# Kernel optimization log

Hardware: AMD Instinct MI355X
Metric: run time of the kernel (lower is better)

The kernel has to match this reference:

```python
import jax, jax.numpy as jnp
import numpy as np

GROUPS = 8
EPS = 1e-5


def group_norm(x, gamma, beta):
    b, c, h, w = x.shape
    xg = x.reshape(b, GROUPS, c // GROUPS, h, w)
    mu = jnp.mean(xg, axis=(2, 3, 4), keepdims=True)
    var = jnp.mean((xg - mu) ** 2, axis=(2, 3, 4), keepdims=True)
    xn = ((xg - mu) * jax.lax.rsqrt(var + EPS)).reshape(b, c, h, w)
    return xn * gamma[None, :, None, None] + beta[None, :, None, None]


def setup_inputs() -> dict:
    key = jax.random.key(0)
    ks = jax.random.split(key, 4)
    b, c, h, w = 4, 64, 64, 64
    x = jax.random.normal(ks[0], (b, c, h, w), dtype=jnp.float32)
    gamma = jnp.ones((c,), dtype=jnp.float32)
    beta = jnp.zeros((c,), dtype=jnp.float32)
    w_qkv = jax.random.normal(ks[1], (3 * c, c), dtype=jnp.float32) * (1.0 / np.sqrt(c))
    b_qkv = jnp.zeros((3 * c,), dtype=jnp.float32)
    w_proj = jax.random.normal(ks[2], (c, c), dtype=jnp.float32) * (1.0 / np.sqrt(c))
    b_proj = jnp.zeros((c,), dtype=jnp.float32)
    return {"x": x, "gamma": gamma, "beta": beta, "w_qkv": w_qkv,
            "b_qkv": b_qkv, "w_proj": w_proj, "b_proj": b_proj}


def reference(x, gamma, beta, w_qkv, b_qkv, w_proj, b_proj):
    b, c, h, w = x.shape
    xn = group_norm(x, gamma, beta)
    # 1x1 conv == per-pixel linear: [b,3c,h,w]
    qkv = jnp.einsum('oc,bchw->bohw', w_qkv, xn) + b_qkv[None, :, None, None]
    q, k, v = jnp.split(qkv, 3, axis=1)
    # flatten spatial -> tokens: [b, hw, c]
    def tok(t):
        return t.reshape(b, c, h * w).transpose(0, 2, 1)
    q, k, v = tok(q), tok(k), tok(v)
    scale = c ** (-0.5)
    attn = jnp.einsum('bqc,bkc->bqk', q, k) * scale  # [b, hw, hw]
    attn = jax.nn.softmax(attn, axis=-1)
    out = jnp.einsum('bqk,bkc->bqc', attn, v)  # [b, hw, c]
    out = out.transpose(0, 2, 1).reshape(b, c, h, w)
    out = jnp.einsum('oc,bchw->bohw', w_proj, out) + b_proj[None, :, None, None]
    return out + x
```

## Files before the change

### kernel.cpp

```cpp
#include <hip/hip_runtime.h>

typedef __bf16 bf16x8 __attribute__((ext_vector_type(8)));
typedef __bf16 bf16x4 __attribute__((ext_vector_type(4)));
typedef float  f32x4  __attribute__((ext_vector_type(4)));

#define GLD_LDS16(gsrc, ldst) \
  __builtin_amdgcn_global_load_lds((const __attribute__((address_space(1))) void*)(gsrc), \
                                   (__attribute__((address_space(3))) void*)(ldst), 16, 0, 0)

__global__ __launch_bounds__(256) void gn_partial_k(const float* __restrict__ x,
                                                    float* __restrict__ partial) {
  __shared__ float red[2][4];
  const int t = threadIdx.x;
  const float4* base = (const float4*)(x + (size_t)blockIdx.x * 4096);
  float s = 0.f, sq = 0.f;
#pragma unroll
  for (int kk = 0; kk < 4; ++kk) {
    float4 v = base[t + kk * 256];
    s  += (v.x + v.y) + (v.z + v.w);
    sq += (v.x * v.x + v.y * v.y) + (v.z * v.z + v.w * v.w);
  }
#pragma unroll
  for (int o = 32; o >= 1; o >>= 1) {
    s  += __shfl_down(s, o, 64);
    sq += __shfl_down(sq, o, 64);
  }
  if ((t & 63) == 0) { red[0][t >> 6] = s; red[1][t >> 6] = sq; }
  __syncthreads();
  if (t == 0) {
    float S  = (red[0][0] + red[0][1]) + (red[0][2] + red[0][3]);
    float SQ = (red[1][0] + red[1][1]) + (red[1][2] + red[1][3]);
    partial[blockIdx.x * 2]     = S;
    partial[blockIdx.x * 2 + 1] = SQ;
  }
}

__global__ void gn_final_k(const float* __restrict__ partial, float* __restrict__ stats) {
  const int t = threadIdx.x;
  if (t < 32) {
    float S = 0.f, SQ = 0.f;
#pragma unroll
    for (int i = 0; i < 8; ++i) {
      S  += partial[(t * 8 + i) * 2];
      SQ += partial[(t * 8 + i) * 2 + 1];
    }
    float mean = S * (1.f / 32768.f);
    float var  = SQ * (1.f / 32768.f) - mean * mean;
    stats[t * 2]     = mean;
    stats[t * 2 + 1] = rsqrtf(fmaxf(var, 0.f) + 1e-5f);
  }
}

__global__ __launch_bounds__(192) void qkv_k(const float* __restrict__ x,
                                             const float* __restrict__ stats,
                                             const float* __restrict__ gamma,
                                             const float* __restrict__ beta,
                                             const float* __restrict__ w_qkv,
                                             const float* __restrict__ b_qkv,
                                             __bf16* __restrict__ qo,
                                             __bf16* __restrict__ ko,
                                             __bf16* __restrict__ vto) {
  __shared__ float xn_lds[32 * 68];
  __shared__ float v_lds[64 * 33];
  const int t  = threadIdx.x;
  const int b  = blockIdx.x >> 7;
  const int s0 = (blockIdx.x & 127) * 32;

  for (int idx = t; idx < 2048; idx += 192) {
    int c = idx >> 5, px = idx & 31;
    float v  = x[((size_t)(b * 64 + c)) * 4096 + s0 + px];
    int   g2 = (b * 8 + (c >> 3)) * 2;
    xn_lds[px * 68 + c] = (v - stats[g2]) * stats[g2 + 1] * gamma[c] + beta[c];
  }
  float4 wr[16];
  const float4* wrow = (const float4*)(w_qkv + t * 64);
#pragma unroll
  for (int i = 0; i < 16; ++i) wr[i] = wrow[i];
  const float bias = b_qkv[t];
  __syncthreads();

  for (int px = 0; px < 32; ++px) {
    const float4* xr = (const float4*)&xn_lds[px * 68];
    float a0 = bias, a1 = 0.f, a2 = 0.f, a3 = 0.f;
#pragma unroll
    for (int i = 0; i < 16; i += 4) {
      float4 x0 = xr[i], x1 = xr[i + 1], x2 = xr[i + 2], x3 = xr[i + 3];
      a0 += wr[i    ].x * x0.x + wr[i    ].y * x0.y + wr[i    ].z * x0.z + wr[i    ].w * x0.w;
      a1 += wr[i + 1].x * x1.x + wr[i + 1].y * x1.y + wr[i + 1].z * x1.z + wr[i + 1].w * x1.w;
      a2 += wr[i + 2].x * x2.x + wr[i + 2].y * x2.y + wr[i + 2].z * x2.z + wr[i + 2].w * x2.w;
      a3 += wr[i + 3].x * x3.x + wr[i + 3].y * x3.y + wr[i + 3].z * x3.z + wr[i + 3].w * x3.w;
    }
    float acc = (a0 + a1) + (a2 + a3);
    if (t < 64)
      qo[((size_t)b * 4096 + s0 + px) * 64 + t] = (__bf16)(acc * 0.125f);
    else if (t < 128)
      ko[((size_t)b * 4096 + s0 + px) * 64 + (t - 64)] = (__bf16)acc;
    else
      v_lds[(t - 128) * 33 + px] = acc;
  }
  __syncthreads();
  for (int u = t; u < 2048; u += 192) {
    int rowc = u >> 5, px = u & 31;
    vto[((size_t)(b * 64 + rowc)) * 4096 + s0 + px] = (__bf16)v_lds[rowc * 33 + px];
  }
}

__global__ __launch_bounds__(512, 2) void attn_k(const __bf16* __restrict__ q,
                                                 const __bf16* __restrict__ k,
                                                 const __bf16* __restrict__ vt,
                                                 __bf16* __restrict__ opart,
                                                 float* __restrict__ mlpart) {
  __shared__ __bf16 k_lds[3][4096];
  __shared__ __bf16 v_lds[3][4096];
  __shared__ __bf16 p_lds[8][2048];
  const int tid  = threadIdx.x;
  const int lane = tid & 63, w = tid >> 6;
  const int row  = lane & 15, grp = lane >> 4;

  const int blk  = blockIdx.x;
  const int xcd  = blk & 7;
  const int b    = xcd >> 1;
  const int rest = blk >> 3;
  const int seg  = rest >> 3;
  const int qblk = (rest & 7) | ((xcd & 1) << 3);
  const int q0   = qblk * 256 + w * 32;
  const int j0b  = seg * 512;

  const __bf16* qp = q  + (size_t)b * 4096 * 64;
  const __bf16* kp = k  + (size_t)b * 4096 * 64;
  const __bf16* vp = vt + (size_t)b * 64 * 4096;

  bf16x8 qf[2][2];
#pragma unroll
  for (int rt = 0; rt < 2; ++rt)
#pragma unroll
    for (int kc = 0; kc < 2; ++kc)
      qf[rt][kc] = *(const bf16x8*)(qp + (size_t)(q0 + rt * 16 + row) * 64 + kc * 32 + grp * 8);
  __builtin_amdgcn_sched_barrier(0);

  f32x4 acc[2][4];
#pragma unroll
  for (int rt = 0; rt < 2; ++rt)
#pragma unroll
    for (int dt = 0; dt < 4; ++dt) acc[rt][dt] = (f32x4){0.f, 0.f, 0.f, 0.f};
  float m[2] = {-1e30f, -1e30f}, l[2] = {0.f, 0.f};

  const int soff = tid * 16;
  const int sj = soff >> 7;
  const int sc = ((soff >> 4) & 7) ^ (sj & 7);

  auto stage = [&](int buf, int j0) {
    GLD_LDS16(kp + (size_t)(j0 + sj) * 64 + sc * 8, (char*)(&k_lds[buf][0]) + soff);
    GLD_LDS16(vp + (size_t)sj * 4096 + j0 + sc * 8, (char*)(&v_lds[buf][0]) + soff);
  };

  stage(0, j0b);
  stage(1, j0b + 64);

  char* const pbase = (char*)&p_lds[w][0];
  const int swz = (row & 7) << 3;

#pragma unroll
  for (int kt = 0; kt < 8; ++kt) {
    const int cur = kt % 3;
    if (kt < 6) stage((kt + 2) % 3, j0b + (kt + 2) * 64);

    if (kt < 6)       asm volatile("s_waitcnt vmcnt(4)" ::: "memory");
    else if (kt == 6) asm volatile("s_waitcnt vmcnt(2)" ::: "memory");
    else              asm volatile("s_waitcnt vmcnt(0)" ::: "memory");
    __builtin_amdgcn_s_barrier();

    const char* kbase = (const char*)&k_lds[cur][0];
    const char* vbase = (const char*)&v_lds[cur][0];

    f32x4 sa[2][4];
#pragma unroll
    for (int rt = 0; rt < 2; ++rt)
#pragma unroll
      for (int jt = 0; jt < 4; ++jt) sa[rt][jt] = (f32x4){0.f, 0.f, 0.f, 0.f};
    __builtin_amdgcn_s_setprio(1);
#pragma unroll
    for (int jt = 0; jt < 4; ++jt) {
      const int jr = jt * 16 + row;
      bf16x8 kf0 = *(const bf16x8*)(kbase + jr * 128 + ((grp ^ (row & 7)) << 4));
      bf16x8 kf1 = *(const bf16x8*)(kbase + jr * 128 + (((4 + grp) ^ (row & 7)) << 4));
      sa[0][jt] = __builtin_amdgcn_mfma_f32_16x16x32_bf16(kf0, qf[0][0], sa[0][jt], 0, 0, 0);
      sa[1][jt] = __builtin_amdgcn_mfma_f32_16x16x32_bf16(kf0, qf[1][0], sa[1][jt], 0, 0, 0);
      sa[0][jt] = __builtin_amdgcn_mfma_f32_16x16x32_bf16(kf1, qf[0][1], sa[0][jt], 0, 0, 0);
      sa[1][jt] = __builtin_amdgcn_mfma_f32_16x16x32_bf16(kf1, qf[1][1], sa[1][jt], 0, 0, 0);
    }
    __builtin_amdgcn_s_setprio(0);

#pragma unroll
    for (int rt = 0; rt < 2; ++rt) {
      float t0 = fmaxf(fmaxf(sa[rt][0][0], sa[rt][0][1]), fmaxf(sa[rt][0][2], sa[rt][0][3]));
      float t1 = fmaxf(fmaxf(sa[rt][1][0], sa[rt][1][1]), fmaxf(sa[rt][1][2], sa[rt][1][3]));
      float t2 = fmaxf(fmaxf(sa[rt][2][0], sa[rt][2][1]), fmaxf(sa[rt][2][2], sa[rt][2][3]));
      float t3 = fmaxf(fmaxf(sa[rt][3][0], sa[rt][3][1]), fmaxf(sa[rt][3][2], sa[rt][3][3]));
      float tmax = fmaxf(fmaxf(t0, t1), fmaxf(t2, t3));
      tmax = fmaxf(tmax, __shfl_xor(tmax, 16, 64));
      tmax = fmaxf(tmax, __shfl_xor(tmax, 32, 64));
      float mn = fmaxf(m[rt], tmax);
      float sf = __expf(m[rt] - mn);
      m[rt] = mn;
      float ls = 0.f;
#pragma unroll
      for (int jt = 0; jt < 4; ++jt) {
        float p0 = __expf(sa[rt][jt][0] - mn);
        float p1 = __expf(sa[rt][jt][1] - mn);
        float p2 = __expf(sa[rt][jt][2] - mn);
        float p3 = __expf(sa[rt][jt][3] - mn);
        ls += (p0 + p1) + (p2 + p3);
        bf16x4 pv = {(__bf16)p0, (__bf16)p1, (__bf16)p2, (__bf16)p3};
        *(bf16x4*)(pbase + ((rt * 16 + row) << 7) + ((((grp << 2) + (jt << 4)) ^ swz) << 1)) = pv;
      }
      l[rt] = l[rt] * sf + ls;
#pragma unroll
      for (int dt = 0; dt < 4; ++dt) {
        acc[rt][dt][0] *= sf; acc[rt][dt][1] *= sf;
        acc[rt][dt][2] *= sf; acc[rt][dt][3] *= sf;
      }
    }
    asm volatile("s_waitcnt lgkmcnt(0)" ::: "memory");

    __builtin_amdgcn_s_setprio(1);
#pragma unroll
    for (int kc = 0; kc < 2; ++kc) {
      const int koff = (((kc << 5) + (grp << 3)) ^ swz) << 1;
      bf16x8 af0 = *(const bf16x8*)(pbase + (row << 7) + koff);
      bf16x8 af1 = *(const bf16x8*)(pbase + ((16 + row) << 7) + koff);
#pragma unroll
      for (int dt = 0; dt < 4; ++dt) {
        const int dr = dt * 16 + row;
        bf16x8 vf = *(const bf16x8*)(vbase + dr * 128 + ((((kc << 2) + grp) ^ (row & 7)) << 4));
        acc[0][dt] = __builtin_amdgcn_mfma_f32_16x16x32_bf16(vf, af0, acc[0][dt], 0, 0, 0);
        acc[1][dt] = __builtin_amdgcn_mfma_f32_16x16x32_bf16(vf, af1, acc[1][dt], 0, 0, 0);
      }
    }
    __builtin_amdgcn_s_setprio(0);

    if (kt < 7) __builtin_amdgcn_s_barrier();
  }

#pragma unroll
  for (int rt = 0; rt < 2; ++rt) {
    float lt = l[rt];
    lt += __shfl_xor(lt, 16, 64);
    lt += __shfl_xor(lt, 32, 64);
    const int qrow = q0 + rt * 16 + row;
    __bf16* ob = opart + ((size_t)(b * 8 + seg) * 4096 + qrow) * 64;
#pragma unroll
    for (int dt = 0; dt < 4; ++dt) {
      bf16x4 ov = {(__bf16)acc[rt][dt][0], (__bf16)acc[rt][dt][1],
                   (__bf16)acc[rt][dt][2], (__bf16)acc[rt][dt][3]};
      *(bf16x4*)(ob + dt * 16 + grp * 4) = ov;
    }
    if (grp == 0) {
      float2 mlv; mlv.x = m[rt]; mlv.y = lt;
      *(float2*)(mlpart + ((size_t)(b * 8 + seg) * 4096 + qrow) * 2) = mlv;
    }
  }
}

__global__ __launch_bounds__(256) void proj_k(const __bf16* __restrict__ opart,
                                              const float* __restrict__ mlpart,
                                              const float* __restrict__ x,
                                              const float* __restrict__ w_proj,
                                              const float* __restrict__ b_proj,
                                              float* __restrict__ out) {
  __shared__ float wseg[8][32];
  __shared__ float a_lds[32 * 68];
  __shared__ float o_lds[64 * 33];
  const int t  = threadIdx.x;
  const int b  = blockIdx.x >> 7;
  const int s0 = (blockIdx.x & 127) * 32;

  if (t < 32) {
    const int rowg = s0 + t;
    float ms[8], ls[8], es[8];
    float M = -1e30f;
#pragma unroll
    for (int s = 0; s < 8; ++s) {
      float2 ml = *(const float2*)(mlpart + ((size_t)(b * 8 + s) * 4096 + rowg) * 2);
      ms[s] = ml.x; ls[s] = ml.y;
      M = fmaxf(M, ms[s]);
    }
    float L = 0.f;
#pragma unroll
    for (int s = 0; s < 8; ++s) { es[s] = __expf(ms[s] - M); L += es[s] * ls[s]; }
    float invL = 1.f / L;
#pragma unroll
    for (int s = 0; s < 8; ++s) wseg[s][t] = es[s] * invL;
  }
  __syncthreads();

  for (int i = t; i < 512; i += 256) {
    const int px = i >> 4, c4 = i & 15;
    const __bf16* obase = opart + ((size_t)(b * 8) * 4096 + s0 + px) * 64 + c4 * 4;
    float4 a = {0.f, 0.f, 0.f, 0.f};
#pragma unroll
    for (int s = 0; s < 8; ++s) {
      bf16x4 v = *(const bf16x4*)(obase + (size_t)s * 4096 * 64);
      float wv = wseg[s][px];
      a.x += wv * (float)v[0]; a.y += wv * (float)v[1];
      a.z += wv * (float)v[2]; a.w += wv * (float)v[3];
    }
    *(float4*)(&a_lds[px * 68 + c4 * 4]) = a;
  }

  const int o = t & 63, wg = t >> 6;
  float4 wr[16];
  const float4* wrow = (const float4*)(w_proj + o * 64);
#pragma unroll
  for (int i = 0; i < 16; ++i) wr[i] = wrow[i];
  const float bias = b_proj[o];
  __syncthreads();

  for (int pp = 0; pp < 8; ++pp) {
    const int px = wg * 8 + pp;
    const float4* ar = (const float4*)&a_lds[px * 68];
    float a0 = bias, a1 = 0.f, a2 = 0.f, a3 = 0.f;
#pragma unroll
    for (int i = 0; i < 16; i += 4) {
      float4 x0 = ar[i], x1 = ar[i + 1], x2 = ar[i + 2], x3 = ar[i + 3];
      a0 += wr[i    ].x * x0.x + wr[i    ].y * x0.y + wr[i    ].z * x0.z + wr[i    ].w * x0.w;
      a1 += wr[i + 1].x * x1.x + wr[i + 1].y * x1.y + wr[i + 1].z * x1.z + wr[i + 1].w * x1.w;
      a2 += wr[i + 2].x * x2.x + wr[i + 2].y * x2.y + wr[i + 2].z * x2.z + wr[i + 2].w * x2.w;
      a3 += wr[i + 3].x * x3.x + wr[i + 3].y * x3.y + wr[i + 3].z * x3.z + wr[i + 3].w * x3.w;
    }
    o_lds[o * 33 + px] = (a0 + a1) + (a2 + a3);
  }
  __syncthreads();
  for (int idx = t; idx < 2048; idx += 256) {
    const int c = idx >> 5, px = idx & 31;
    const size_t gi = ((size_t)(b * 64 + c)) * 4096 + s0 + px;
    out[gi] = o_lds[c * 33 + px] + x[gi];
  }
}

extern "C" void kernel_launch(void* const* d_in, const int* in_sizes, int n_in,
                              void* d_out, int out_size, void* d_ws, size_t ws_size,
                              hipStream_t stream) {
  const float* x      = (const float*)d_in[0];
  const float* gamma  = (const float*)d_in[1];
  const float* beta   = (const float*)d_in[2];
  const float* w_qkv  = (const float*)d_in[3];
  const float* b_qkv  = (const float*)d_in[4];
  const float* w_proj = (const float*)d_in[5];
  const float* b_proj = (const float*)d_in[6];
  float* out = (float*)d_out;

  char* ws = (char*)d_ws;
  float*  partial = (float*)ws;
  float*  stats   = partial + 512;
  __bf16* qb  = (__bf16*)(ws + 4096);
  __bf16* kb  = qb  + (size_t)4 * 4096 * 64;
  __bf16* vtb = kb  + (size_t)4 * 4096 * 64;
  __bf16* opart = vtb + (size_t)4 * 4096 * 64;
  float*  mlpart = (float*)(opart + (size_t)4 * 8 * 4096 * 64);

  gn_partial_k<<<256, 256, 0, stream>>>(x, partial);
  gn_final_k<<<1, 64, 0, stream>>>(partial, stats);
  qkv_k<<<512, 192, 0, stream>>>(x, stats, gamma, beta, w_qkv, b_qkv, qb, kb, vtb);
  attn_k<<<512, 512, 0, stream>>>(qb, kb, vtb, opart, mlpart);
  proj_k<<<512, 256, 0, stream>>>(opart, mlpart, x, w_proj, b_proj, out);
}
```

Measured before the change: 80.38 us.

## Switch attention to 32x32 MFMA with register-resident P via permlane swaps

Rewrites the attention inner loop to use 32x32x16 bf16 MFMA tiles. The softmax probabilities stay in registers and are rearranged into the operand layout with v_cvt_pk_bf16 and v_permlane32_swap, which removes the per-wave P round trip through LDS and the lgkmcnt wait. Q is pre-scaled by log2(e)/8 so exp2f can replace __expf, and proj_k's segment merge now uses exp2f to match. The barrier is moved before staging so one barrier per iteration suffices, at the cost of a shallower vmcnt prefetch window.

```diff
diff --git a/kernel.cpp b/kernel.cpp
--- a/kernel.cpp
+++ b/kernel.cpp
@@ -3,10 +3,26 @@
 typedef __bf16 bf16x8 __attribute__((ext_vector_type(8)));
 typedef __bf16 bf16x4 __attribute__((ext_vector_type(4)));
 typedef float  f32x4  __attribute__((ext_vector_type(4)));
+typedef float  f32x16 __attribute__((ext_vector_type(16)));
 
 #define GLD_LDS16(gsrc, ldst) \
   __builtin_amdgcn_global_load_lds((const __attribute__((address_space(1))) void*)(gsrc), \
                                    (__attribute__((address_space(3))) void*)(ldst), 16, 0, 0)
+
+__device__ inline unsigned cvt_pk_bf16(float lo, float hi) {
+  unsigned r;
+  asm("v_cvt_pk_bf16_f32 %0, %1, %2" : "=v"(r) : "v"(lo), "v"(hi));
+  return r;
+}
+__device__ inline void pl32_swap(unsigned& a, unsigned& b) {
+  asm volatile("v_permlane32_swap_b32 %0, %1" : "+v"(a), "+v"(b));
+}
+__device__ inline f32x16 zero16() {
+  f32x16 z;
+#pragma unroll
+  for (int i = 0; i < 16; ++i) z[i] = 0.f;
+  return z;
+}
 
 __global__ __launch_bounds__(256) void gn_partial_k(const float* __restrict__ x,
                                                     float* __restrict__ partial) {
@@ -92,7 +108,7 @@
     }
     float acc = (a0 + a1) + (a2 + a3);
     if (t < 64)
-      qo[((size_t)b * 4096 + s0 + px) * 64 + t] = (__bf16)(acc * 0.125f);
+      qo[((size_t)b * 4096 + s0 + px) * 64 + t] = (__bf16)(acc * 0.18033688f);
     else if (t < 128)
       ko[((size_t)b * 4096 + s0 + px) * 64 + (t - 64)] = (__bf16)acc;
     else
@@ -112,10 +128,12 @@
                                                  float* __restrict__ mlpart) {
   __shared__ __bf16 k_lds[3][4096];
   __shared__ __bf16 v_lds[3][4096];
-  __shared__ __bf16 p_lds[8][2048];
+
   const int tid  = threadIdx.x;
   const int lane = tid & 63, w = tid >> 6;
-  const int row  = lane & 15, grp = lane >> 4;
+  const int col  = lane & 31;
+  const int h    = lane >> 5;
+  const int swz  = col & 7;
 
   const int blk  = blockIdx.x;
   const int xcd  = blk & 7;
@@ -130,20 +148,14 @@
   const __bf16* kp = k  + (size_t)b * 4096 * 64;
   const __bf16* vp = vt + (size_t)b * 64 * 4096;
 
-  bf16x8 qf[2][2];
-#pragma unroll
-  for (int rt = 0; rt < 2; ++rt)
-#pragma unroll
-    for (int kc = 0; kc < 2; ++kc)
-      qf[rt][kc] = *(const bf16x8*)(qp + (size_t)(q0 + rt * 16 + row) * 64 + kc * 32 + grp * 8);
+  bf16x8 qf[4];
+#pragma unroll
+  for (int kk = 0; kk < 4; ++kk)
+    qf[kk] = *(const bf16x8*)(qp + (size_t)(q0 + col) * 64 + kk * 16 + h * 8);
   __builtin_amdgcn_sched_barrier(0);
 
-  f32x4 acc[2][4];
-#pragma unroll
-  for (int rt = 0; rt < 2; ++rt)
-#pragma unroll
-    for (int dt = 0; dt < 4; ++dt) acc[rt][dt] = (f32x4){0.f, 0.f, 0.f, 0.f};
-  float m[2] = {-1e30f, -1e30f}, l[2] = {0.f, 0.f};
+  f32x16 acc0 = zero16(), acc1 = zero16();
+  float m = -1e30f, l = 0.f;
 
   const int soff = tid * 16;
   const int sj = soff >> 7;
@@ -157,108 +169,98 @@
   stage(0, j0b);
   stage(1, j0b + 64);
 
-  char* const pbase = (char*)&p_lds[w][0];
-  const int swz = (row & 7) << 3;
-
 #pragma unroll
   for (int kt = 0; kt < 8; ++kt) {
-    const int cur = kt % 3;
+    if (kt < 7) asm volatile("s_waitcnt vmcnt(2)" ::: "memory");
+    else        asm volatile("s_waitcnt vmcnt(0)" ::: "memory");
+    __builtin_amdgcn_s_barrier();
+
     if (kt < 6) stage((kt + 2) % 3, j0b + (kt + 2) * 64);
 
-    if (kt < 6)       asm volatile("s_waitcnt vmcnt(4)" ::: "memory");
-    else if (kt == 6) asm volatile("s_waitcnt vmcnt(2)" ::: "memory");
-    else              asm volatile("s_waitcnt vmcnt(0)" ::: "memory");
-    __builtin_amdgcn_s_barrier();
-
-    const char* kbase = (const char*)&k_lds[cur][0];
-    const char* vbase = (const char*)&v_lds[cur][0];
-
-    f32x4 sa[2][4];
-#pragma unroll
-    for (int rt = 0; rt < 2; ++rt)
-#pragma unroll
-      for (int jt = 0; jt < 4; ++jt) sa[rt][jt] = (f32x4){0.f, 0.f, 0.f, 0.f};
+    const char* kbase = (const char*)&k_lds[kt % 3][0];
+    const char* vbase = (const char*)&v_lds[kt % 3][0];
+
+    f32x16 sa0 = zero16(), sa1 = zero16();
     __builtin_amdgcn_s_setprio(1);
 #pragma unroll
-    for (int jt = 0; jt < 4; ++jt) {
-      const int jr = jt * 16 + row;
-      bf16x8 kf0 = *(const bf16x8*)(kbase + jr * 128 + ((grp ^ (row & 7)) << 4));
-      bf16x8 kf1 = *(const bf16x8*)(kbase + jr * 128 + (((4 + grp) ^ (row & 7)) << 4));
-      sa[0][jt] = __builtin_amdgcn_mfma_f32_16x16x32_bf16(kf0, qf[0][0], sa[0][jt], 0, 0, 0);
-      sa[1][jt] = __builtin_amdgcn_mfma_f32_16x16x32_bf16(kf0, qf[1][0], sa[1][jt], 0, 0, 0);
-      sa[0][jt] = __builtin_amdgcn_mfma_f32_16x16x32_bf16(kf1, qf[0][1], sa[0][jt], 0, 0, 0);
-      sa[1][jt] = __builtin_amdgcn_mfma_f32_16x16x32_bf16(kf1, qf[1][1], sa[1][jt], 0, 0, 0);
+    for (int kk = 0; kk < 4; ++kk) {
+      bf16x8 kf0 = *(const bf16x8*)(kbase + col * 128        + (((2 * kk + h) ^ swz) << 4));
+      bf16x8 kf1 = *(const bf16x8*)(kbase + (32 + col) * 128 + (((2 * kk + h) ^ swz) << 4));
+      sa0 = __builtin_amdgcn_mfma_f32_32x32x16_bf16(kf0, qf[kk], sa0, 0, 0, 0);
+      sa1 = __builtin_amdgcn_mfma_f32_32x32x16_bf16(kf1, qf[kk], sa1, 0, 0, 0);
     }
     __builtin_amdgcn_s_setprio(0);
 
-#pragma unroll
-    for (int rt = 0; rt < 2; ++rt) {
-      float t0 = fmaxf(fmaxf(sa[rt][0][0], sa[rt][0][1]), fmaxf(sa[rt][0][2], sa[rt][0][3]));
-      float t1 = fmaxf(fmaxf(sa[rt][1][0], sa[rt][1][1]), fmaxf(sa[rt][1][2], sa[rt][1][3]));
-      float t2 = fmaxf(fmaxf(sa[rt][2][0], sa[rt][2][1]), fmaxf(sa[rt][2][2], sa[rt][2][3]));
-      float t3 = fmaxf(fmaxf(sa[rt][3][0], sa[rt][3][1]), fmaxf(sa[rt][3][2], sa[rt][3][3]));
-      float tmax = fmaxf(fmaxf(t0, t1), fmaxf(t2, t3));
-      tmax = fmaxf(tmax, __shfl_xor(tmax, 16, 64));
-      tmax = fmaxf(tmax, __shfl_xor(tmax, 32, 64));
-      float mn = fmaxf(m[rt], tmax);
-      float sf = __expf(m[rt] - mn);
-      m[rt] = mn;
-      float ls = 0.f;
-#pragma unroll
-      for (int jt = 0; jt < 4; ++jt) {
-        float p0 = __expf(sa[rt][jt][0] - mn);
-        float p1 = __expf(sa[rt][jt][1] - mn);
-        float p2 = __expf(sa[rt][jt][2] - mn);
-        float p3 = __expf(sa[rt][jt][3] - mn);
-        ls += (p0 + p1) + (p2 + p3);
-        bf16x4 pv = {(__bf16)p0, (__bf16)p1, (__bf16)p2, (__bf16)p3};
-        *(bf16x4*)(pbase + ((rt * 16 + row) << 7) + ((((grp << 2) + (jt << 4)) ^ swz) << 1)) = pv;
-      }
-      l[rt] = l[rt] * sf + ls;
-#pragma unroll
-      for (int dt = 0; dt < 4; ++dt) {
-        acc[rt][dt][0] *= sf; acc[rt][dt][1] *= sf;
-        acc[rt][dt][2] *= sf; acc[rt][dt][3] *= sf;
-      }
-    }
-    asm volatile("s_waitcnt lgkmcnt(0)" ::: "memory");
+    float x0 = fmaxf(fmaxf(sa0[0], sa0[1]),   fmaxf(sa0[2], sa0[3]));
+    float x1 = fmaxf(fmaxf(sa0[4], sa0[5]),   fmaxf(sa0[6], sa0[7]));
+    float x2 = fmaxf(fmaxf(sa0[8], sa0[9]),   fmaxf(sa0[10], sa0[11]));
+    float x3 = fmaxf(fmaxf(sa0[12], sa0[13]), fmaxf(sa0[14], sa0[15]));
+    float y0 = fmaxf(fmaxf(sa1[0], sa1[1]),   fmaxf(sa1[2], sa1[3]));
+    float y1 = fmaxf(fmaxf(sa1[4], sa1[5]),   fmaxf(sa1[6], sa1[7]));
+    float y2 = fmaxf(fmaxf(sa1[8], sa1[9]),   fmaxf(sa1[10], sa1[11]));
+    float y3 = fmaxf(fmaxf(sa1[12], sa1[13]), fmaxf(sa1[14], sa1[15]));
+    float mx = fmaxf(fmaxf(fmaxf(x0, x1), fmaxf(x2, x3)),
+                     fmaxf(fmaxf(y0, y1), fmaxf(y2, y3)));
+    mx = fmaxf(mx, __shfl_xor(mx, 32, 64));
+    float mn = fmaxf(m, mx);
+    float sf = exp2f(m - mn);
+    m = mn;
+    float ls = 0.f;
+#pragma unroll
+    for (int r = 0; r < 16; ++r) { sa0[r] = exp2f(sa0[r] - mn); ls += sa0[r]; }
+#pragma unroll
+    for (int r = 0; r < 16; ++r) { sa1[r] = exp2f(sa1[r] - mn); ls += sa1[r]; }
+    l = l * sf + ls;
+    acc0 *= sf;
+    acc1 *= sf;
+
+    unsigned w0[8], w1[8];
+#pragma unroll
+    for (int qd = 0; qd < 4; ++qd) {
+      w0[qd * 2]     = cvt_pk_bf16(sa0[4 * qd],     sa0[4 * qd + 1]);
+      w0[qd * 2 + 1] = cvt_pk_bf16(sa0[4 * qd + 2], sa0[4 * qd + 3]);
+      w1[qd * 2]     = cvt_pk_bf16(sa1[4 * qd],     sa1[4 * qd + 1]);
+      w1[qd * 2 + 1] = cvt_pk_bf16(sa1[4 * qd + 2], sa1[4 * qd + 3]);
+    }
+    bf16x8 pa[4];
+#pragma unroll
+    for (int c = 0; c < 4; ++c) {
+      const unsigned* wt = (c < 2) ? w0 : w1;
+      unsigned a0 = wt[(2 * (c & 1)) * 2],     b0 = wt[(2 * (c & 1) + 1) * 2];
+      unsigned a1 = wt[(2 * (c & 1)) * 2 + 1], b1 = wt[(2 * (c & 1) + 1) * 2 + 1];
+      pl32_swap(a0, b0);
+      pl32_swap(a1, b1);
+      uint4 u; u.x = a0; u.y = a1; u.z = b0; u.w = b1;
+      pa[c] = __builtin_bit_cast(bf16x8, u);
+    }
 
     __builtin_amdgcn_s_setprio(1);
 #pragma unroll
-    for (int kc = 0; kc < 2; ++kc) {
-      const int koff = (((kc << 5) + (grp << 3)) ^ swz) << 1;
-      bf16x8 af0 = *(const bf16x8*)(pbase + (row << 7) + koff);
-      bf16x8 af1 = *(const bf16x8*)(pbase + ((16 + row) << 7) + koff);
-#pragma unroll
-      for (int dt = 0; dt < 4; ++dt) {
-        const int dr = dt * 16 + row;
-        bf16x8 vf = *(const bf16x8*)(vbase + dr * 128 + ((((kc << 2) + grp) ^ (row & 7)) << 4));
-        acc[0][dt] = __builtin_amdgcn_mfma_f32_16x16x32_bf16(vf, af0, acc[0][dt], 0, 0, 0);
-        acc[1][dt] = __builtin_amdgcn_mfma_f32_16x16x32_bf16(vf, af1, acc[1][dt], 0, 0, 0);
-      }
+    for (int c = 0; c < 4; ++c) {
+      bf16x8 vf0 = *(const bf16x8*)(vbase + col * 128        + (((2 * c + h) ^ swz) << 4));
+      bf16x8 vf1 = *(const bf16x8*)(vbase + (32 + col) * 128 + (((2 * c + h) ^ swz) << 4));
+      acc0 = __builtin_amdgcn_mfma_f32_32x32x16_bf16(vf0, pa[c], acc0, 0, 0, 0);
+      acc1 = __builtin_amdgcn_mfma_f32_32x32x16_bf16(vf1, pa[c], acc1, 0, 0, 0);
     }
     __builtin_amdgcn_s_setprio(0);
-
-    if (kt < 7) __builtin_amdgcn_s_barrier();
-  }
-
-#pragma unroll
-  for (int rt = 0; rt < 2; ++rt) {
-    float lt = l[rt];
-    lt += __shfl_xor(lt, 16, 64);
-    lt += __shfl_xor(lt, 32, 64);
-    const int qrow = q0 + rt * 16 + row;
-    __bf16* ob = opart + ((size_t)(b * 8 + seg) * 4096 + qrow) * 64;
-#pragma unroll
-    for (int dt = 0; dt < 4; ++dt) {
-      bf16x4 ov = {(__bf16)acc[rt][dt][0], (__bf16)acc[rt][dt][1],
-                   (__bf16)acc[rt][dt][2], (__bf16)acc[rt][dt][3]};
-      *(bf16x4*)(ob + dt * 16 + grp * 4) = ov;
-    }
-    if (grp == 0) {
-      float2 mlv; mlv.x = m[rt]; mlv.y = lt;
-      *(float2*)(mlpart + ((size_t)(b * 8 + seg) * 4096 + qrow) * 2) = mlv;
-    }
+  }
+
+  float lf = l + __shfl_xor(l, 32, 64);
+  const int qrow = q0 + col;
+  __bf16* ob = opart + ((size_t)(b * 8 + seg) * 4096 + qrow) * 64;
+#pragma unroll
+  for (int rq = 0; rq < 4; ++rq) {
+    const int d0 = 8 * rq + 4 * h;
+    bf16x4 o0 = {(__bf16)acc0[4 * rq], (__bf16)acc0[4 * rq + 1],
+                 (__bf16)acc0[4 * rq + 2], (__bf16)acc0[4 * rq + 3]};
+    bf16x4 o1 = {(__bf16)acc1[4 * rq], (__bf16)acc1[4 * rq + 1],
+                 (__bf16)acc1[4 * rq + 2], (__bf16)acc1[4 * rq + 3]};
+    *(bf16x4*)(ob + d0)      = o0;
+    *(bf16x4*)(ob + 32 + d0) = o1;
+  }
+  if (h == 0) {
+    float2 mlv; mlv.x = m; mlv.y = lf;
+    *(float2*)(mlpart + ((size_t)(b * 8 + seg) * 4096 + qrow) * 2) = mlv;
   }
 }
 
@@ -287,7 +289,7 @@
     }
     float L = 0.f;
 #pragma unroll
-    for (int s = 0; s < 8; ++s) { es[s] = __expf(ms[s] - M); L += es[s] * ls[s]; }
+    for (int s = 0; s < 8; ++s) { es[s] = exp2f(ms[s] - M); L += es[s] * ls[s]; }
     float invL = 1.f / L;
 #pragma unroll
     for (int s = 0; s < 8; ++s) wseg[s][t] = es[s] * invL;
```

New measurement: 80.37 us. About the same (-0.0%).
